# Kernel tuning notes

Hardware: AMD Instinct MI355X
Metric: run time of the kernel (lower is better)

## Reference

```python
import jax, jax.numpy as jnp
import numpy as np

B, N, C, H = 128, 256, 512, 2
HD = C // H  # head_dim == num_patches == N by construction of the module's einsums
ALPHA = 3.0


def _safe_pow(x, p):
    # x >= 0 (post-relu); avoid 0**p corner issues while matching x**p exactly for x>0
    pos = x > 0
    return jnp.where(pos, jnp.where(pos, x, 1.0) ** p, 0.0)


def setup_inputs() -> dict:
    key = jax.random.key(0)
    ks = jax.random.split(key, 12)
    s = 0.02
    return {
        "x": jax.random.normal(ks[0], (B, N, C), jnp.float32),
        "Wq": jax.random.normal(ks[1], (C, C), jnp.float32) * s,
        "bq": jnp.zeros((C,), jnp.float32),
        "Wk": jax.random.normal(ks[2], (C, C), jnp.float32) * s,
        "bk": jnp.zeros((C,), jnp.float32),
        "Wvs": jax.random.normal(ks[3], (C, C // 2), jnp.float32) * s,
        "bvs": jnp.zeros((C // 2,), jnp.float32),
        "Wvc": jax.random.normal(ks[4], (C, C // 2), jnp.float32) * s,
        "bvc": jnp.zeros((C // 2,), jnp.float32),
        "power": jnp.ones((1, H, 1, HD), jnp.float32),
        "W_s": jax.random.uniform(ks[5], (N, HD // 2), jnp.float32),
        "W_c": jax.random.uniform(ks[6], (N, HD // 2), jnp.float32),
        "Wp": jax.random.normal(ks[7], (C, C), jnp.float32) * s,
        "bp": jnp.zeros((C,), jnp.float32),
    }


def reference(x, Wq, bq, Wk, bk, Wvs, bvs, Wvc, bvc, power, W_s, W_c, Wp, bp):
    b, n, c = x.shape
    h, hd = H, c // H
    # projections -> [B, H, N, hd] (or hd//2 for values)
    q = (x @ Wq + bq).reshape(b, n, h, hd).transpose(0, 2, 1, 3)
    k = (x @ Wk + bk).reshape(b, n, h, hd).transpose(0, 2, 1, 3)
    v_s = (x @ Wvs + bvs).reshape(b, n, h, hd // 2).transpose(0, 2, 1, 3)
    v_c = (x @ Wvc + bvc).reshape(b, n, h, hd // 2).transpose(0, 2, 1, 3)

    power_val = 1.0 + ALPHA * jax.nn.sigmoid(power)  # [1,H,1,hd]
    q_pos = _safe_pow(jax.nn.relu(q), power_val)
    q_neg = _safe_pow(jax.nn.relu(-q), power_val)
    k_pos = _safe_pow(jax.nn.relu(k), power_val)
    k_neg = _safe_pow(jax.nn.relu(-k), power_val)

    # kv_s = einsum(k_pos,v_s)+einsum(k_neg,v_s) == einsum(k_pos+k_neg, v_s); same for kv_c
    k_abs = k_pos + k_neg
    q_abs = q_pos + q_neg
    kv_s = jnp.einsum('bhnj,bhjd->bhnd', k_abs, v_s)
    q_s_context = jnp.einsum('bhni,bhid->bhnd', q_abs, kv_s)
    kv_c = jnp.einsum('bhnj,bhjd->bhnd', k_abs, v_c)
    q_c_context = jnp.einsum('bhni,bhid->bhnd', q_abs, kv_c)

    kp_sum = k_pos.sum(-1)  # [B,H,N]
    kn_sum = k_neg.sum(-1)
    denom_s = jnp.einsum('bhni,bhi->bhn', q_pos, kp_sum) + jnp.einsum('bhni,bhi->bhn', q_neg, kn_sum)
    denom_c = jnp.einsum('bhni,bhi->bhn', q_pos, kn_sum) + jnp.einsum('bhni,bhi->bhn', q_neg, kp_sum)

    attn_s = q_s_context / (denom_s[..., None] + 1e-6) * W_s  # W_s: [N, hd//2]
    attn_c = q_c_context / (denom_c[..., None] + 1e-6) * W_c

    out = jnp.concatenate([attn_s, attn_c], axis=-1)  # [B,H,N,hd]
    out = out.transpose(0, 2, 1, 3).reshape(b, n, c)
    return out @ Wp + bp
```

## Files before the change

### kernel.cpp

```cpp
#include <hip/hip_runtime.h>
#include <hip/hip_bf16.h>
#include <math.h>

typedef unsigned int u32;
typedef short bf16x8 __attribute__((ext_vector_type(8)));
typedef float f32x4 __attribute__((ext_vector_type(4)));
typedef u32 u32x4 __attribute__((ext_vector_type(4)));

__device__ __forceinline__ float bf2f(short s) {
    u32 u = ((u32)(unsigned short)s) << 16;
    return __builtin_bit_cast(float, u);
}
__device__ __forceinline__ short f2bf(float f) {
    u32 u = __builtin_bit_cast(u32, f);
    u32 r = u + 0x7fffu + ((u >> 16) & 1u);
    return (short)(r >> 16);
}
__device__ __forceinline__ float fast_log2(float x) {
    float r; asm volatile("v_log_f32 %0, %1" : "=v"(r) : "v"(x)); return r;
}
__device__ __forceinline__ float fast_exp2(float x) {
    float r; asm volatile("v_exp_f32 %0, %1" : "=v"(r) : "v"(x)); return r;
}
__device__ __forceinline__ void gload_lds16(const short* g, short* lds) {
    __builtin_amdgcn_global_load_lds(
        (const __attribute__((address_space(1))) u32*)g,
        (__attribute__((address_space(3))) u32*)lds, 16, 0, 0);
}
__device__ __forceinline__ bf16x8 stripsign(bf16x8 v) {
    u32x4 u = __builtin_bit_cast(u32x4, v);
    u &= 0x7fff7fffu;
    return __builtin_bit_cast(bf16x8, u);
}

struct P {
    const float* bcat; const float* pcol;
    short* qa; short* ka;
    short* vt; short* kvt;
    const float* dsb; const float* dcb; const float* Ws; const float* Wc;
    short* Y; float* out;
};

__global__ void k_pack(const float* __restrict__ Wq, const float* __restrict__ Wk,
                       const float* __restrict__ Wvs, const float* __restrict__ Wvc,
                       const float* __restrict__ Wp,
                       const float* __restrict__ bq, const float* __restrict__ bk,
                       const float* __restrict__ bvs, const float* __restrict__ bvc,
                       const float* __restrict__ bp, const float* __restrict__ power,
                       short* __restrict__ WcatT, float* __restrict__ bcat, float* __restrict__ pcol)
{
    int i = blockIdx.x * 256 + threadIdx.x;
    int r = i >> 9, k = i & 511;
    float w;
    if (r < 512)       w = Wq[k * 512 + r];
    else if (r < 1024) w = Wk[k * 512 + (r - 512)];
    else if (r < 1536) {
        int rr = r - 1024; int h = rr >> 8; int d = rr & 255;
        w = (d < 128) ? Wvs[k * 256 + h * 128 + d] : Wvc[k * 256 + h * 128 + (d - 128)];
    } else             w = Wp[k * 512 + (r - 1536)];
    WcatT[i] = f2bf(w);

    if (i < 2048) {
        float bb;
        if (i < 512)       bb = bq[i];
        else if (i < 1024) bb = bk[i - 512];
        else if (i < 1536) {
            int rr = i - 1024; int h = rr >> 8; int d = rr & 255;
            bb = (d < 128) ? bvs[h * 128 + d] : bvc[h * 128 + (d - 128)];
        } else             bb = bp[i - 1536];
        bcat[i] = bb;
    }
    if (i < 512) pcol[i] = 1.0f + 3.0f / (1.0f + expf(-power[i]));
}

__global__ void k_cast(const float* __restrict__ x, short* __restrict__ xb)
{
    int i = blockIdx.x * 256 + threadIdx.x;
    float4 v = ((const float4*)x)[i];
    short4 s;
    s.x = f2bf(v.x); s.y = f2bf(v.y); s.z = f2bf(v.z); s.w = f2bf(v.w);
    ((short4*)xb)[i] = s;
}

__global__ void k_ksum(const short* __restrict__ ka,
                       float* __restrict__ kpsum, float* __restrict__ knsum)
{
    int gid = blockIdx.x * 256 + threadIdx.x;
    int gw = gid >> 6;
    int lane = gid & 63;
    short4 a4 = ((const short4*)(ka + ((size_t)gw << 8)))[lane];
    short aa[4] = {a4.x, a4.y, a4.z, a4.w};
    float sp = 0.f, sn = 0.f;
#pragma unroll
    for (int j = 0; j < 4; ++j) {
        float a = fabsf(bf2f(aa[j]));
        if (((unsigned short)aa[j] >> 15) == 0) sp += a; else sn += a;
    }
#pragma unroll
    for (int m = 1; m < 64; m <<= 1) { sp += __shfl_xor(sp, m, 64); sn += __shfl_xor(sn, m, 64); }
    if (lane == 0) { kpsum[gw] = sp; knsum[gw] = sn; }
}

__global__ void k_denom(const short* __restrict__ qa,
                        const float* __restrict__ kpsum, const float* __restrict__ knsum,
                        float* __restrict__ dsb, float* __restrict__ dcb)
{
    int gid = blockIdx.x * 256 + threadIdx.x;
    int gw = gid >> 6;
    int lane = gid & 63;
    int bhl = gw >> 8;
    short4 q4 = ((const short4*)(qa + ((size_t)gw << 8)))[lane];
    float4 kp4 = ((const float4*)(kpsum + ((size_t)bhl << 8)))[lane];
    float4 kn4 = ((const float4*)(knsum + ((size_t)bhl << 8)))[lane];
    short qq[4] = {q4.x, q4.y, q4.z, q4.w};
    float kp[4] = {kp4.x, kp4.y, kp4.z, kp4.w};
    float kn[4] = {kn4.x, kn4.y, kn4.z, kn4.w};
    float ss = 0.f, sc = 0.f;
#pragma unroll
    for (int j = 0; j < 4; ++j) {
        float a = fabsf(bf2f(qq[j]));
        if (((unsigned short)qq[j] >> 15) == 0) { ss += a * kp[j]; sc += a * kn[j]; }
        else                                    { ss += a * kn[j]; sc += a * kp[j]; }
    }
#pragma unroll
    for (int m = 1; m < 64; m <<= 1) { ss += __shfl_xor(ss, m, 64); sc += __shfl_xor(sc, m, 64); }
    if (lane == 0) { dsb[gw] = ss; dcb[gw] = sc; }
}

#define MODE_QK  0
#define MODE_VT  1
#define MODE_KV  2
#define MODE_CTX 3
#define MODE_OUT 4

template <int MODE>
__launch_bounds__(256, 4)
__global__ void gemm_nt(const short* __restrict__ Ag, const short* __restrict__ Bg,
                        int K, int tilesN, P p)
{
    __shared__ __align__(16) short sm[16384];
    short* As = sm;
    short* Bs = sm + 8192;

    const int nwg = gridDim.x * gridDim.y;
    const int s = blockIdx.y * gridDim.x + blockIdx.x;
    const int cpx = nwg >> 3;
    const int lin = (s & 7) * cpx + (s >> 3);

    int tm, tn, bhl;
    if (MODE == MODE_KV || MODE == MODE_CTX) {
        bhl = lin >> 2;
        int rem = lin & 3;
        tm = rem / tilesN; tn = rem % tilesN;
    } else {
        bhl = 0;
        tm = lin / tilesN; tn = lin % tilesN;
    }

    const short* A = Ag;
    const short* B = Bg;
    if (MODE == MODE_KV || MODE == MODE_CTX) {
        A += (size_t)bhl << 16;
        B += (size_t)bhl << 16;
    }
    constexpr bool stripA = (MODE == MODE_CTX);
    constexpr bool stripB = (MODE == MODE_KV);

    const int t = threadIdx.x;
    const int lane = t & 63;
    const int w = t >> 6;
    const int wr = w >> 1, wc = w & 1;

    f32x4 acc[4][4];
#pragma unroll
    for (int i = 0; i < 4; ++i)
#pragma unroll
        for (int j = 0; j < 4; ++j) acc[i][j] = 0.f;

    const int nkt = K >> 6;
    for (int kt = 0; kt < nkt; ++kt) {
#pragma unroll
        for (int q4i = 0; q4i < 4; ++q4i) {
            int seg = w * 4 + q4i;
            int r = seg * 8 + (lane >> 3);
            int c = (lane & 7) ^ (r & 7);
            gload_lds16(A + (size_t)(tm * 128 + r) * K + kt * 64 + c * 8, &As[seg * 512]);
            gload_lds16(B + (size_t)(tn * 128 + r) * K + kt * 64 + c * 8, &Bs[seg * 512]);
        }
        __syncthreads();
#pragma unroll
        for (int kk = 0; kk < 2; ++kk) {
            bf16x8 af[4], bfr[4];
#pragma unroll
            for (int mt = 0; mt < 4; ++mt) {
                int row = wr * 64 + mt * 16 + (lane & 15);
                int ch = kk * 4 + (lane >> 4);
                af[mt] = *(const bf16x8*)(&As[row * 64 + ((ch ^ (row & 7)) << 3)]);
                if constexpr (stripA) af[mt] = stripsign(af[mt]);
            }
#pragma unroll
            for (int nt = 0; nt < 4; ++nt) {
                int row = wc * 64 + nt * 16 + (lane & 15);
                int ch = kk * 4 + (lane >> 4);
                bfr[nt] = *(const bf16x8*)(&Bs[row * 64 + ((ch ^ (row & 7)) << 3)]);
                if constexpr (stripB) bfr[nt] = stripsign(bfr[nt]);
            }
#pragma unroll
            for (int mt = 0; mt < 4; ++mt)
#pragma unroll
                for (int nt = 0; nt < 4; ++nt)
                    acc[mt][nt] = __builtin_amdgcn_mfma_f32_16x16x32_bf16(af[mt], bfr[nt], acc[mt][nt], 0, 0, 0);
        }
        __syncthreads();
    }

    if (MODE == MODE_QK || MODE == MODE_VT) {
#pragma unroll
        for (int mt = 0; mt < 4; ++mt) {
#pragma unroll
            for (int nt = 0; nt < 4; ++nt) {
#pragma unroll
                for (int r = 0; r < 4; ++r) {
                    int lrow = wr * 64 + mt * 16 + (lane >> 4) * 4 + r;
                    int lcol = wc * 64 + nt * 16 + (lane & 15);
                    float v = acc[mt][nt][r];
                    short sv;
                    if (MODE == MODE_QK) {
                        int col_g = tn * 128 + lcol;
                        v += p.bcat[col_g];
                        float pw = p.pcol[col_g & 511];
                        float a = (v != 0.0f) ? fast_exp2(pw * fast_log2(fabsf(v))) : 0.0f;
                        unsigned short sa = (unsigned short)f2bf(a);
                        sa |= (unsigned short)((__builtin_bit_cast(u32, v) >> 16) & 0x8000u);
                        sv = (short)sa;
                    } else {
                        v += p.bcat[1024 + tm * 128 + lrow];
                        sv = f2bf(v);
                    }
                    int g = lcol >> 3;
                    sm[lrow * 128 + ((g ^ (lrow & 7)) << 3) + (lcol & 7)] = sv;
                }
            }
        }
        __syncthreads();
#pragma unroll
        for (int i = 0; i < 8; ++i) {
            int slot = i * 256 + t;
            int lrow = slot >> 4;
            int g = slot & 15;
            bf16x8 val = *(const bf16x8*)&sm[lrow * 128 + ((g ^ (lrow & 7)) << 3)];
            if (MODE == MODE_QK) {
                int row_g = tm * 128 + lrow;
                int col0 = tn * 128 + g * 8;
                int bl = row_g >> 8, n = row_g & 255;
                int h = (col0 >> 8) & 1;
                short* dst = (col0 < 512) ? p.qa : p.ka;
                *(bf16x8*)(dst + (((size_t)((bl * 2 + h) * 256 + n)) << 8) + (col0 & 255)) = val;
            } else {
                int d_g = tm * 128 + lrow;
                int col0 = tn * 128 + g * 8;
                int h = d_g >> 8, d = d_g & 255;
                int bl = col0 >> 8, n0 = col0 & 255;
                *(bf16x8*)(p.vt + (((size_t)((bl * 2 + h) * 256 + d)) << 8) + n0) = val;
            }
        }
    } else if (MODE == MODE_OUT) {
        float* smf = (float*)sm;
#pragma unroll
        for (int half = 0; half < 2; ++half) {
            if (wr == half) {
#pragma unroll
                for (int mt = 0; mt < 4; ++mt) {
#pragma unroll
                    for (int nt = 0; nt < 4; ++nt) {
#pragma unroll
                        for (int r = 0; r < 4; ++r) {
                            int lrow = mt * 16 + (lane >> 4) * 4 + r;
                            int lcol = wc * 64 + nt * 16 + (lane & 15);
                            float v = acc[mt][nt][r] + p.bcat[1536 + tn * 128 + lcol];
                            int g = lcol >> 2;
                            smf[lrow * 128 + ((g ^ (lrow & 7)) << 2) + (lcol & 3)] = v;
                        }
                    }
                }
            }
            __syncthreads();
#pragma unroll
            for (int i = 0; i < 8; ++i) {
                int slot = i * 256 + t;
                int lrow = slot >> 5;
                int g = slot & 31;
                float4 val = *(const float4*)&smf[lrow * 128 + ((g ^ (lrow & 7)) << 2)];
                int row_g = tm * 128 + half * 64 + lrow;
                *(float4*)(p.out + ((size_t)row_g << 9) + tn * 128 + g * 4) = val;
            }
            __syncthreads();
        }
    } else {
#pragma unroll
        for (int mt = 0; mt < 4; ++mt) {
#pragma unroll
            for (int nt = 0; nt < 4; ++nt) {
#pragma unroll
                for (int r = 0; r < 4; ++r) {
                    int lrow = wr * 64 + mt * 16 + (lane >> 4) * 4 + r;
                    int lcol = wc * 64 + nt * 16 + (lane & 15);
                    float v = acc[mt][nt][r];
                    short sv;
                    if (MODE == MODE_KV) {
                        sv = f2bf(v);
                    } else {
                        int n = tm * 128 + lrow, d = tn * 128 + lcol;
                        float den = ((d < 128) ? p.dsb : p.dcb)[bhl * 256 + n] + 1e-6f;
                        float wgt = (d < 128) ? p.Ws[n * 128 + d] : p.Wc[n * 128 + (d - 128)];
                        sv = f2bf(v / den * wgt);
                    }
                    int g = lcol >> 3;
                    sm[lrow * 128 + ((g ^ (lrow & 7)) << 3) + (lcol & 7)] = sv;
                }
            }
        }
        __syncthreads();
#pragma unroll
        for (int i = 0; i < 8; ++i) {
            int slot = i * 256 + t;
            int lrow = slot >> 4;
            int g = slot & 15;
            bf16x8 val = *(const bf16x8*)&sm[lrow * 128 + ((g ^ (lrow & 7)) << 3)];
            int row = tm * 128 + lrow;
            int col0 = tn * 128 + g * 8;
            if (MODE == MODE_KV) {
                *(bf16x8*)(p.kvt + ((size_t)bhl << 16) + (row << 8) + col0) = val;
            } else {
                int bl = bhl >> 1, h = bhl & 1;
                *(bf16x8*)(p.Y + ((size_t)(bl * 256 + row) << 9) + h * 256 + col0) = val;
            }
        }
    }
}

extern "C" void kernel_launch(void* const* d_in, const int* in_sizes, int n_in,
                              void* d_out, int out_size, void* d_ws, size_t ws_size,
                              hipStream_t stream)
{
    const float* x     = (const float*)d_in[0];
    const float* Wq    = (const float*)d_in[1];
    const float* bq    = (const float*)d_in[2];
    const float* Wk    = (const float*)d_in[3];
    const float* bk    = (const float*)d_in[4];
    const float* Wvs   = (const float*)d_in[5];
    const float* bvs   = (const float*)d_in[6];
    const float* Wvc   = (const float*)d_in[7];
    const float* bvc   = (const float*)d_in[8];
    const float* power = (const float*)d_in[9];
    const float* Ws    = (const float*)d_in[10];
    const float* Wc    = (const float*)d_in[11];
    const float* Wp    = (const float*)d_in[12];
    const float* bp    = (const float*)d_in[13];
    (void)in_sizes; (void)n_in; (void)out_size; (void)ws_size;

    char* ws = (char*)d_ws;
    size_t off = 0;
    auto alloc = [&](size_t bytes) { void* pp = ws + off; off += (bytes + 255) & ~(size_t)255; return pp; };
    short* Wcat = (short*)alloc(2097152);
    float* bcat = (float*)alloc(8192);
    float* pcol = (float*)alloc(2048);
    short* xb   = (short*)alloc(33554432);
    short* qa   = (short*)alloc(33554432);
    short* ka   = (short*)alloc(33554432);
    short* vt   = (short*)alloc(33554432);
    short* kvt  = (short*)alloc(33554432);
    float* kpsum= (float*)alloc(262144);
    float* knsum= (float*)alloc(262144);
    float* dsb  = (float*)alloc(262144);
    float* dcb  = (float*)alloc(262144);

    P p{};
    p.bcat = bcat; p.pcol = pcol;
    p.qa = qa; p.ka = ka;
    p.vt = vt; p.kvt = kvt;
    p.dsb = dsb; p.dcb = dcb; p.Ws = Ws; p.Wc = Wc;
    p.Y = xb; p.out = nullptr;

    k_pack<<<4096, 256, 0, stream>>>(Wq, Wk, Wvs, Wvc, Wp, bq, bk, bvs, bvc, bp, power, Wcat, bcat, pcol);

    k_cast<<<16384, 256, 0, stream>>>(x, xb);

    gemm_nt<MODE_QK><<<dim3(2048, 1), 256, 0, stream>>>(xb, Wcat, 512, 8, p);

    gemm_nt<MODE_VT><<<dim3(1024, 1), 256, 0, stream>>>(Wcat + 1024 * 512, xb, 512, 256, p);

    gemm_nt<MODE_KV><<<dim3(4, 256), 256, 0, stream>>>(vt, ka, 256, 2, p);

    k_ksum<<<16384, 256, 0, stream>>>(ka, kpsum, knsum);
    k_denom<<<16384, 256, 0, stream>>>(qa, kpsum, knsum, dsb, dcb);

    gemm_nt<MODE_CTX><<<dim3(4, 256), 256, 0, stream>>>(qa, kvt, 256, 2, p);

    P po = p;
    po.out = (float*)d_out;
    gemm_nt<MODE_OUT><<<dim3(1024, 1), 256, 0, stream>>>(xb, Wcat + 1536 * 512, 512, 4, po);
}
```

Baseline: 207.3 us.

## Add 256x256 double-buffered 8-wave GEMM for projection and output stages

Adds a new gemm8 kernel with 512 threads and 256x256 output tiles. It double-buffers LDS and interleaves the global-to-LDS prefetch of the next K tile with MFMA work, using barriers and s_setprio. The QK, VT and output projection GEMMs now use it, and gemm_nt is reduced to the batched KV/CTX paths. Larger tiles raise data reuse and cut the number of workgroups, at the cost of 128KB of LDS per block, high register use and fewer blocks for load balancing.

```diff
diff --git a/kernel.cpp b/kernel.cpp
--- a/kernel.cpp
+++ b/kernel.cpp
@@ -134,6 +134,218 @@
 #define MODE_OUT 4
 
 template <int MODE>
+__launch_bounds__(512, 2)
+__global__ void gemm8(const short* __restrict__ Ag, const short* __restrict__ Bg,
+                      int tilesN, P p)
+{
+    __shared__ __align__(16) short sm[65536];
+
+    const int nwg = gridDim.x;
+    const int s0 = blockIdx.x;
+    const int cpx = nwg >> 3;
+    const int lin = (s0 & 7) * cpx + (s0 >> 3);
+    const int tm = lin / tilesN, tn = lin % tilesN;
+
+    const int t = threadIdx.x;
+    const int lane = t & 63;
+    const int w = t >> 6;
+    const int wr = w >> 2;
+    const int wc = w & 3;
+
+    const short* A = Ag + (size_t)tm * 256 * 512;
+    const short* B = Bg + (size_t)tn * 256 * 512;
+
+    auto stage_half = [&](const short* G, short* tile, int h, int kt) {
+#pragma unroll
+        for (int q = 0; q < 2; ++q) {
+            int u = q * 512 + t;
+            int lr = u >> 3, pp = u & 7;
+            int g = pp ^ (lr & 7);
+            gload_lds16(G + (size_t)(h * 128 + lr) * 512 + kt * 64 + g * 8,
+                        tile + h * 8192 + (q * 512 + w * 64) * 8);
+        }
+    };
+    auto lda = [&](bf16x8* a, const short* At, int kk, int mh) {
+#pragma unroll
+        for (int m2 = 0; m2 < 4; ++m2) {
+            int row = wr * 128 + mh * 64 + m2 * 16 + (lane & 15);
+            int ch = kk * 4 + (lane >> 4);
+            a[m2] = *(const bf16x8*)(At + row * 64 + ((ch ^ (row & 7)) << 3));
+        }
+    };
+    auto ldb = [&](bf16x8* b, const short* Bt, int kk) {
+#pragma unroll
+        for (int nf = 0; nf < 4; ++nf) {
+            int row = wc * 64 + nf * 16 + (lane & 15);
+            int ch = kk * 4 + (lane >> 4);
+            b[nf] = *(const bf16x8*)(Bt + row * 64 + ((ch ^ (row & 7)) << 3));
+        }
+    };
+
+    f32x4 acc[8][4];
+#pragma unroll
+    for (int i = 0; i < 8; ++i)
+#pragma unroll
+        for (int j = 0; j < 4; ++j) acc[i][j] = 0.f;
+
+    stage_half(A, sm, 0, 0); stage_half(A, sm, 1, 0);
+    stage_half(B, sm + 16384, 0, 0); stage_half(B, sm + 16384, 1, 0);
+    asm volatile("s_waitcnt vmcnt(0)" ::: "memory");
+    __builtin_amdgcn_sched_barrier(0);
+    __builtin_amdgcn_s_barrier();
+
+    for (int kt = 0; kt < 8; ++kt) {
+        const short* At = sm + (kt & 1) * 32768;
+        const short* Bt = At + 16384;
+        short* An = sm + ((kt + 1) & 1) * 32768;
+        short* Bn = An + 16384;
+        const bool pf = (kt + 1) < 8;
+        bf16x8 a[4], b[4];
+
+        lda(a, At, 0, 0); ldb(b, Bt, 0);
+        if (pf) stage_half(A, An, 0, kt + 1);
+        __builtin_amdgcn_s_barrier();
+        asm volatile("s_waitcnt lgkmcnt(0)" ::: "memory");
+        __builtin_amdgcn_sched_barrier(0);
+        __builtin_amdgcn_s_setprio(1);
+#pragma unroll
+        for (int m2 = 0; m2 < 4; ++m2)
+#pragma unroll
+            for (int nf = 0; nf < 4; ++nf)
+                acc[m2][nf] = __builtin_amdgcn_mfma_f32_16x16x32_bf16(a[m2], b[nf], acc[m2][nf], 0, 0, 0);
+        __builtin_amdgcn_s_setprio(0);
+        __builtin_amdgcn_s_barrier();
+
+        lda(a, At, 0, 1);
+        if (pf) stage_half(B, Bn, 0, kt + 1);
+        __builtin_amdgcn_s_barrier();
+        asm volatile("s_waitcnt lgkmcnt(0)" ::: "memory");
+        __builtin_amdgcn_sched_barrier(0);
+        __builtin_amdgcn_s_setprio(1);
+#pragma unroll
+        for (int m2 = 0; m2 < 4; ++m2)
+#pragma unroll
+            for (int nf = 0; nf < 4; ++nf)
+                acc[4 + m2][nf] = __builtin_amdgcn_mfma_f32_16x16x32_bf16(a[m2], b[nf], acc[4 + m2][nf], 0, 0, 0);
+        __builtin_amdgcn_s_setprio(0);
+        __builtin_amdgcn_s_barrier();
+
+        lda(a, At, 1, 0); ldb(b, Bt, 1);
+        if (pf) stage_half(A, An, 1, kt + 1);
+        __builtin_amdgcn_s_barrier();
+        asm volatile("s_waitcnt lgkmcnt(0)" ::: "memory");
+        __builtin_amdgcn_sched_barrier(0);
+        __builtin_amdgcn_s_setprio(1);
+#pragma unroll
+        for (int m2 = 0; m2 < 4; ++m2)
+#pragma unroll
+            for (int nf = 0; nf < 4; ++nf)
+                acc[m2][nf] = __builtin_amdgcn_mfma_f32_16x16x32_bf16(a[m2], b[nf], acc[m2][nf], 0, 0, 0);
+        __builtin_amdgcn_s_setprio(0);
+        __builtin_amdgcn_s_barrier();
+
+        lda(a, At, 1, 1);
+        if (pf) stage_half(B, Bn, 1, kt + 1);
+        __builtin_amdgcn_s_barrier();
+        asm volatile("s_waitcnt lgkmcnt(0)" ::: "memory");
+        __builtin_amdgcn_sched_barrier(0);
+        __builtin_amdgcn_s_setprio(1);
+#pragma unroll
+        for (int m2 = 0; m2 < 4; ++m2)
+#pragma unroll
+            for (int nf = 0; nf < 4; ++nf)
+                acc[4 + m2][nf] = __builtin_amdgcn_mfma_f32_16x16x32_bf16(a[m2], b[nf], acc[4 + m2][nf], 0, 0, 0);
+        __builtin_amdgcn_s_setprio(0);
+        asm volatile("s_waitcnt vmcnt(0)" ::: "memory");
+        __builtin_amdgcn_sched_barrier(0);
+        __builtin_amdgcn_s_barrier();
+    }
+
+    if (MODE == MODE_QK || MODE == MODE_VT) {
+#pragma unroll
+        for (int mf = 0; mf < 8; ++mf) {
+#pragma unroll
+            for (int nf = 0; nf < 4; ++nf) {
+#pragma unroll
+                for (int r = 0; r < 4; ++r) {
+                    int lrow = wr * 128 + mf * 16 + (lane >> 4) * 4 + r;
+                    int lcol = wc * 64 + nf * 16 + (lane & 15);
+                    float v = acc[mf][nf][r];
+                    short sv;
+                    if (MODE == MODE_QK) {
+                        int col_g = tn * 256 + lcol;
+                        v += p.bcat[col_g];
+                        float pw = p.pcol[col_g & 511];
+                        float aa = (v != 0.0f) ? fast_exp2(pw * fast_log2(fabsf(v))) : 0.0f;
+                        unsigned short sa = (unsigned short)f2bf(aa);
+                        sa |= (unsigned short)((__builtin_bit_cast(u32, v) >> 16) & 0x8000u);
+                        sv = (short)sa;
+                    } else {
+                        v += p.bcat[1024 + tm * 256 + lrow];
+                        sv = f2bf(v);
+                    }
+                    int g = lcol >> 3;
+                    sm[lrow * 256 + ((g ^ (lrow & 7)) << 3) + (lcol & 7)] = sv;
+                }
+            }
+        }
+        __syncthreads();
+#pragma unroll
+        for (int i = 0; i < 16; ++i) {
+            int slot = i * 512 + t;
+            int lrow = slot >> 5;
+            int g = slot & 31;
+            bf16x8 val = *(const bf16x8*)&sm[lrow * 256 + ((g ^ (lrow & 7)) << 3)];
+            int col0 = tn * 256 + g * 8;
+            if (MODE == MODE_QK) {
+                int row_g = tm * 256 + lrow;
+                int bl = row_g >> 8, n = row_g & 255;
+                int h = (col0 >> 8) & 1;
+                short* dst = (col0 < 512) ? p.qa : p.ka;
+                *(bf16x8*)(dst + (((size_t)((bl * 2 + h) * 256 + n)) << 8) + (col0 & 255)) = val;
+            } else {
+                int d_g = tm * 256 + lrow;
+                int h = d_g >> 8, d = d_g & 255;
+                int bl = col0 >> 8, n0 = col0 & 255;
+                *(bf16x8*)(p.vt + (((size_t)((bl * 2 + h) * 256 + d)) << 8) + n0) = val;
+            }
+        }
+    } else {
+        float* smf = (float*)sm;
+#pragma unroll
+        for (int half = 0; half < 2; ++half) {
+            if (wr == half) {
+#pragma unroll
+                for (int mf = 0; mf < 8; ++mf) {
+#pragma unroll
+                    for (int nf = 0; nf < 4; ++nf) {
+#pragma unroll
+                        for (int r = 0; r < 4; ++r) {
+                            int lrow = mf * 16 + (lane >> 4) * 4 + r;
+                            int lcol = wc * 64 + nf * 16 + (lane & 15);
+                            float v = acc[mf][nf][r] + p.bcat[1536 + tn * 256 + lcol];
+                            int g = lcol >> 2;
+                            smf[lrow * 256 + ((g ^ (lrow & 7)) << 2) + (lcol & 3)] = v;
+                        }
+                    }
+                }
+            }
+            __syncthreads();
+#pragma unroll
+            for (int i = 0; i < 16; ++i) {
+                int slot = i * 512 + t;
+                int lrow = slot >> 6;
+                int g = slot & 63;
+                float4 val = *(const float4*)&smf[lrow * 256 + ((g ^ (lrow & 7)) << 2)];
+                int row_g = tm * 256 + half * 128 + lrow;
+                *(float4*)(p.out + ((size_t)row_g << 9) + tn * 256 + g * 4) = val;
+            }
+            __syncthreads();
+        }
+    }
+}
+
+template <int MODE>
 __launch_bounds__(256, 4)
 __global__ void gemm_nt(const short* __restrict__ Ag, const short* __restrict__ Bg,
                         int K, int tilesN, P p)
@@ -147,22 +359,12 @@
     const int cpx = nwg >> 3;
     const int lin = (s & 7) * cpx + (s >> 3);
 
-    int tm, tn, bhl;
-    if (MODE == MODE_KV || MODE == MODE_CTX) {
-        bhl = lin >> 2;
-        int rem = lin & 3;
-        tm = rem / tilesN; tn = rem % tilesN;
-    } else {
-        bhl = 0;
-        tm = lin / tilesN; tn = lin % tilesN;
-    }
-
-    const short* A = Ag;
-    const short* B = Bg;
-    if (MODE == MODE_KV || MODE == MODE_CTX) {
-        A += (size_t)bhl << 16;
-        B += (size_t)bhl << 16;
-    }
+    const int bhl = lin >> 2;
+    const int rem = lin & 3;
+    const int tm = rem / tilesN, tn = rem % tilesN;
+
+    const short* A = Ag + ((size_t)bhl << 16);
+    const short* B = Bg + ((size_t)bhl << 16);
     constexpr bool stripA = (MODE == MODE_CTX);
     constexpr bool stripB = (MODE == MODE_KV);
 
@@ -214,127 +416,43 @@
         __syncthreads();
     }
 
-    if (MODE == MODE_QK || MODE == MODE_VT) {
-#pragma unroll
-        for (int mt = 0; mt < 4; ++mt) {
-#pragma unroll
-            for (int nt = 0; nt < 4; ++nt) {
-#pragma unroll
-                for (int r = 0; r < 4; ++r) {
-                    int lrow = wr * 64 + mt * 16 + (lane >> 4) * 4 + r;
-                    int lcol = wc * 64 + nt * 16 + (lane & 15);
-                    float v = acc[mt][nt][r];
-                    short sv;
-                    if (MODE == MODE_QK) {
-                        int col_g = tn * 128 + lcol;
-                        v += p.bcat[col_g];
-                        float pw = p.pcol[col_g & 511];
-                        float a = (v != 0.0f) ? fast_exp2(pw * fast_log2(fabsf(v))) : 0.0f;
-                        unsigned short sa = (unsigned short)f2bf(a);
-                        sa |= (unsigned short)((__builtin_bit_cast(u32, v) >> 16) & 0x8000u);
-                        sv = (short)sa;
-                    } else {
-                        v += p.bcat[1024 + tm * 128 + lrow];
-                        sv = f2bf(v);
-                    }
-                    int g = lcol >> 3;
-                    sm[lrow * 128 + ((g ^ (lrow & 7)) << 3) + (lcol & 7)] = sv;
+#pragma unroll
+    for (int mt = 0; mt < 4; ++mt) {
+#pragma unroll
+        for (int nt = 0; nt < 4; ++nt) {
+#pragma unroll
+            for (int r = 0; r < 4; ++r) {
+                int lrow = wr * 64 + mt * 16 + (lane >> 4) * 4 + r;
+                int lcol = wc * 64 + nt * 16 + (lane & 15);
+                float v = acc[mt][nt][r];
+                short sv;
+                if (MODE == MODE_KV) {
+                    sv = f2bf(v);
+                } else {
+                    int n = tm * 128 + lrow, d = tn * 128 + lcol;
+                    float den = ((d < 128) ? p.dsb : p.dcb)[bhl * 256 + n] + 1e-6f;
+                    float wgt = (d < 128) ? p.Ws[n * 128 + d] : p.Wc[n * 128 + (d - 128)];
+                    sv = f2bf(v / den * wgt);
                 }
-            }
-        }
-        __syncthreads();
-#pragma unroll
-        for (int i = 0; i < 8; ++i) {
-            int slot = i * 256 + t;
-            int lrow = slot >> 4;
-            int g = slot & 15;
-            bf16x8 val = *(const bf16x8*)&sm[lrow * 128 + ((g ^ (lrow & 7)) << 3)];
-            if (MODE == MODE_QK) {
-                int row_g = tm * 128 + lrow;
-                int col0 = tn * 128 + g * 8;
-                int bl = row_g >> 8, n = row_g & 255;
-                int h = (col0 >> 8) & 1;
-                short* dst = (col0 < 512) ? p.qa : p.ka;
-                *(bf16x8*)(dst + (((size_t)((bl * 2 + h) * 256 + n)) << 8) + (col0 & 255)) = val;
-            } else {
-                int d_g = tm * 128 + lrow;
-                int col0 = tn * 128 + g * 8;
-                int h = d_g >> 8, d = d_g & 255;
-                int bl = col0 >> 8, n0 = col0 & 255;
-                *(bf16x8*)(p.vt + (((size_t)((bl * 2 + h) * 256 + d)) << 8) + n0) = val;
-            }
-        }
-    } else if (MODE == MODE_OUT) {
-        float* smf = (float*)sm;
-#pragma unroll
-        for (int half = 0; half < 2; ++half) {
-            if (wr == half) {
-#pragma unroll
-                for (int mt = 0; mt < 4; ++mt) {
-#pragma unroll
-                    for (int nt = 0; nt < 4; ++nt) {
-#pragma unroll
-                        for (int r = 0; r < 4; ++r) {
-                            int lrow = mt * 16 + (lane >> 4) * 4 + r;
-                            int lcol = wc * 64 + nt * 16 + (lane & 15);
-                            float v = acc[mt][nt][r] + p.bcat[1536 + tn * 128 + lcol];
-                            int g = lcol >> 2;
-                            smf[lrow * 128 + ((g ^ (lrow & 7)) << 2) + (lcol & 3)] = v;
-                        }
-                    }
-                }
-            }
-            __syncthreads();
-#pragma unroll
-            for (int i = 0; i < 8; ++i) {
-                int slot = i * 256 + t;
-                int lrow = slot >> 5;
-                int g = slot & 31;
-                float4 val = *(const float4*)&smf[lrow * 128 + ((g ^ (lrow & 7)) << 2)];
-                int row_g = tm * 128 + half * 64 + lrow;
-                *(float4*)(p.out + ((size_t)row_g << 9) + tn * 128 + g * 4) = val;
-            }
-            __syncthreads();
-        }
-    } else {
-#pragma unroll
-        for (int mt = 0; mt < 4; ++mt) {
-#pragma unroll
-            for (int nt = 0; nt < 4; ++nt) {
-#pragma unroll
-                for (int r = 0; r < 4; ++r) {
-                    int lrow = wr * 64 + mt * 16 + (lane >> 4) * 4 + r;
-                    int lcol = wc * 64 + nt * 16 + (lane & 15);
-                    float v = acc[mt][nt][r];
-                    short sv;
-                    if (MODE == MODE_KV) {
-                        sv = f2bf(v);
-                    } else {
-                        int n = tm * 128 + lrow, d = tn * 128 + lcol;
-                        float den = ((d < 128) ? p.dsb : p.dcb)[bhl * 256 + n] + 1e-6f;
-                        float wgt = (d < 128) ? p.Ws[n * 128 + d] : p.Wc[n * 128 + (d - 128)];
-                        sv = f2bf(v / den * wgt);
-                    }
-                    int g = lcol >> 3;
-                    sm[lrow * 128 + ((g ^ (lrow & 7)) << 3) + (lcol & 7)] = sv;
-                }
-            }
-        }
-        __syncthreads();
-#pragma unroll
-        for (int i = 0; i < 8; ++i) {
-            int slot = i * 256 + t;
-            int lrow = slot >> 4;
-            int g = slot & 15;
-            bf16x8 val = *(const bf16x8*)&sm[lrow * 128 + ((g ^ (lrow & 7)) << 3)];
-            int row = tm * 128 + lrow;
-            int col0 = tn * 128 + g * 8;
-            if (MODE == MODE_KV) {
-                *(bf16x8*)(p.kvt + ((size_t)bhl << 16) + (row << 8) + col0) = val;
-            } else {
-                int bl = bhl >> 1, h = bhl & 1;
-                *(bf16x8*)(p.Y + ((size_t)(bl * 256 + row) << 9) + h * 256 + col0) = val;
-            }
+                int g = lcol >> 3;
+                sm[lrow * 128 + ((g ^ (lrow & 7)) << 3) + (lcol & 7)] = sv;
+            }
+        }
+    }
+    __syncthreads();
+#pragma unroll
+    for (int i = 0; i < 8; ++i) {
+        int slot = i * 256 + t;
+        int lrow = slot >> 4;
+        int g = slot & 15;
+        bf16x8 val = *(const bf16x8*)&sm[lrow * 128 + ((g ^ (lrow & 7)) << 3)];
+        int row = tm * 128 + lrow;
+        int col0 = tn * 128 + g * 8;
+        if (MODE == MODE_KV) {
+            *(bf16x8*)(p.kvt + ((size_t)bhl << 16) + (row << 8) + col0) = val;
+        } else {
+            int bl = bhl >> 1, h = bhl & 1;
+            *(bf16x8*)(p.Y + ((size_t)(bl * 256 + row) << 9) + h * 256 + col0) = val;
         }
     }
 }
@@ -386,9 +504,9 @@
 
     k_cast<<<16384, 256, 0, stream>>>(x, xb);
 
-    gemm_nt<MODE_QK><<<dim3(2048, 1), 256, 0, stream>>>(xb, Wcat, 512, 8, p);
-
-    gemm_nt<MODE_VT><<<dim3(1024, 1), 256, 0, stream>>>(Wcat + 1024 * 512, xb, 512, 256, p);
+    gemm8<MODE_QK><<<512, 512, 0, stream>>>(xb, Wcat, 4, p);
+
+    gemm8<MODE_VT><<<256, 512, 0, stream>>>(Wcat + 1024 * 512, xb, 128, p);
 
     gemm_nt<MODE_KV><<<dim3(4, 256), 256, 0, stream>>>(vt, ka, 256, 2, p);
 
@@ -399,5 +517,5 @@
 
     P po = p;
     po.out = (float*)d_out;
-    gemm_nt<MODE_OUT><<<dim3(1024, 1), 256, 0, stream>>>(xb, Wcat + 1536 * 512, 512, 4, po);
-}
+    gemm8<MODE_OUT><<<256, 512, 0, stream>>>(xb, Wcat + 1536 * 512, 2, po);
+}
```

After: 246.1 us. 1.19x slower.
